# Optimization experiments

Hardware: AMD Instinct MI355X
Metric: run time of the kernel (lower is better)

## Reference

```python
import jax, jax.numpy as jnp
import numpy as np
from jax import lax

N, T, IN = 64, 1024, 64
H = 512
H2 = H // 2   # 256
H4 = H // 4   # 128
H10 = H // 10 # 51


def _lstm(x, Wih, Whh, bih, bhh):
    """PyTorch-style LSTM, batch_first. x: [N,T,in]. Returns hs [N,T,h], h_T, c_T."""
    n, t, _ = x.shape
    h = Whh.shape[1]
    b = bih + bhh

    def step(carry, xt):
        hprev, cprev = carry
        gates = xt @ Wih.T + hprev @ Whh.T + b
        i, f, g, o = jnp.split(gates, 4, axis=-1)
        i = jax.nn.sigmoid(i)
        f = jax.nn.sigmoid(f)
        g = jnp.tanh(g)
        o = jax.nn.sigmoid(o)
        c = f * cprev + i * g
        hnew = o * jnp.tanh(c)
        return (hnew, c), hnew

    h0 = jnp.zeros((n, h), x.dtype)
    c0 = jnp.zeros((n, h), x.dtype)
    (hT, cT), hs = lax.scan(step, (h0, c0), x.transpose(1, 0, 2))
    return hs.transpose(1, 0, 2), hT, cT


def _causal_self_attention(hs):
    """Unscaled dot-product causal attention, equivalent to the python loop."""
    n, t, h = hs.shape
    scores = jnp.einsum('nth,nsh->nts', hs, hs)  # [N,T,T]
    mask = jnp.tril(jnp.ones((t, t), bool))
    scores = jnp.where(mask[None], scores, -jnp.inf)
    attn = jax.nn.softmax(scores, axis=-1)
    return jnp.einsum('nts,nsh->nth', attn, hs)


def setup_inputs() -> dict:
    key = jax.random.key(0)
    ks = jax.random.split(key, 16)
    s = 0.05
    return {
        'x': jax.random.normal(ks[0], (N, T, IN), jnp.float32),
        'W_ih1': jax.random.normal(ks[1], (4 * H, IN), jnp.float32) * s,
        'W_hh1': jax.random.normal(ks[2], (4 * H, H), jnp.float32) * s,
        'b_ih1': jax.random.normal(ks[3], (4 * H,), jnp.float32) * s,
        'b_hh1': jax.random.normal(ks[4], (4 * H,), jnp.float32) * s,
        'W_ih2': jax.random.normal(ks[5], (4 * H2, H), jnp.float32) * s,
        'W_hh2': jax.random.normal(ks[6], (4 * H2, H2), jnp.float32) * s,
        'b_ih2': jax.random.normal(ks[7], (4 * H2,), jnp.float32) * s,
        'b_hh2': jax.random.normal(ks[8], (4 * H2,), jnp.float32) * s,
        'fc1_w': jax.random.normal(ks[9], (H4, 2 * H2), jnp.float32) * s,
        'fc1_b': jax.random.normal(ks[10], (H4,), jnp.float32) * s,
        'fc2_w': jax.random.normal(ks[11], (H10, H4), jnp.float32) * s,
        'fc2_b': jax.random.normal(ks[12], (H10,), jnp.float32) * s,
        'fc3_w': jax.random.normal(ks[13], (1, H10), jnp.float32) * s,
        'fc3_b': jax.random.normal(ks[14], (1,), jnp.float32) * s,
    }


def reference(x, W_ih1, W_hh1, b_ih1, b_hh1, W_ih2, W_hh2, b_ih2, b_hh2,
              fc1_w, fc1_b, fc2_w, fc2_b, fc3_w, fc3_b):
    out, h1, c1 = _lstm(x, W_ih1, W_hh1, b_ih1, b_hh1)     # [N,T,H]
    out, h2, c2 = _lstm(out, W_ih2, W_hh2, b_ih2, b_hh2)   # [N,T,H2]
    contexts = _causal_self_attention(out)                  # [N,T,H2]
    out = jnp.concatenate((contexts, out), axis=2)          # [N,T,2*H2]
    out = jax.nn.relu(out @ fc1_w.T + fc1_b)                # dropout_ratio=0 -> identity
    out = jax.nn.relu(out @ fc2_w.T + fc2_b)
    out = out @ fc3_w.T + fc3_b                              # [N,T,1]
    return out, h1, c1, h2, c2
```

## Files before the change

kernel.cpp:

```cpp
#include <hip/hip_runtime.h>
#include <hip/hip_bf16.h>

#define N_   64
#define T_   1024
#define IN_  64
#define H1_  512
#define H2_  256
#define NG   4
#define NU1  16
#define NU2  8
#define RING 8
#define RING2 4
#define SENT 0xAAAAAAAAu

typedef __bf16 bf16x8 __attribute__((ext_vector_type(8)));
typedef float  f32x4  __attribute__((ext_vector_type(4)));
typedef unsigned int u32x4 __attribute__((ext_vector_type(4)));
typedef unsigned short u16x8 __attribute__((ext_vector_type(8)));
typedef unsigned long long u64;
typedef __hip_bfloat16 bf16_t;

#define OFF_FLG2  8192u
#define OFF_QUE   12288u
#define ZERO_BYTES 16384u
#define OFF_H1R   16384u
#define OFF_H2R   540672u
#define OFF_XB    671744u
#define OFF_W1    9060352u
#define OFF_W2    11419648u
#define OFF_B1    12992512u
#define OFF_B2    13000704u
#define OFF_FC1W  13004800u
#define OFF_FC2W  13135872u
#define OFF_HS2   13152256u
#define OFF_BURN  46706688u

__device__ __forceinline__ bf16x8 ld16(const bf16_t* p) {
  u32x4 u = *reinterpret_cast<const u32x4*>(p);
  return __builtin_bit_cast(bf16x8, u);
}
__device__ __forceinline__ u64 ld64_mall(const void* p) {
  return __hip_atomic_load((const u64*)p, __ATOMIC_RELAXED, __HIP_MEMORY_SCOPE_AGENT);
}
__device__ __forceinline__ void st4_mall(bf16_t* p, unsigned v) {
  __hip_atomic_store((unsigned*)p, v, __ATOMIC_RELAXED, __HIP_MEMORY_SCOPE_AGENT);
}
__device__ __forceinline__ unsigned ldflag(unsigned* p) {
  return __hip_atomic_load(p, __ATOMIC_RELAXED, __HIP_MEMORY_SCOPE_AGENT);
}
__device__ __forceinline__ bool sentok(u64 w) {
  return ((unsigned)w != SENT) && ((unsigned)(w >> 32) != SENT);
}
__device__ __forceinline__ f32x4 mfma_bf16(bf16x8 a, bf16x8 b, f32x4 c) {
  return __builtin_amdgcn_mfma_f32_16x16x32_bf16(a, b, c, 0, 0, 0);
}
__device__ __forceinline__ float sigf(float x) { return 1.f / (1.f + __expf(-x)); }
__device__ __forceinline__ float tanh_fast(float x) {
  float e = __expf(-2.f * fabsf(x));
  float r = (1.f - e) / (1.f + e);
  return x < 0.f ? -r : r;
}
__device__ __forceinline__ unsigned short bf16_bits(float v) {
  __hip_bfloat16 b = __float2bfloat16(v);
  return *reinterpret_cast<unsigned short*>(&b);
}

__global__ void setup_kernel(const float* __restrict__ x,
    const float* __restrict__ Wih1, const float* __restrict__ Whh1,
    const float* __restrict__ bih1, const float* __restrict__ bhh1,
    const float* __restrict__ Wih2, const float* __restrict__ Whh2,
    const float* __restrict__ bih2, const float* __restrict__ bhh2,
    const float* __restrict__ fc1w, const float* __restrict__ fc2w,
    char* __restrict__ ws)
{
  bf16_t* xb = (bf16_t*)(ws + OFF_XB);
  bf16_t* w1 = (bf16_t*)(ws + OFF_W1);
  bf16_t* w2 = (bf16_t*)(ws + OFF_W2);
  float*  b1 = (float*)(ws + OFF_B1);
  float*  b2 = (float*)(ws + OFF_B2);
  bf16_t* f1 = (bf16_t*)(ws + OFF_FC1W);
  bf16_t* f2 = (bf16_t*)(ws + OFF_FC2W);
  const long E0 = 4194304, E1 = E0 + 1179648, E2 = E1 + 786432,
             E3 = E2 + 2048, E4 = E3 + 1024, E5 = E4 + 65536, E6 = E5 + 8192;
  for (long i = blockIdx.x * (long)blockDim.x + threadIdx.x; i < E6;
       i += (long)gridDim.x * blockDim.x) {
    if (i < E0) {
      xb[i] = __float2bfloat16(x[i]);
    } else if (i < E1) {
      long idx = i - E0; long j = idx / 576, k = idx % 576;
      float v = (k < 64) ? Wih1[j * 64 + k] : Whh1[j * 512 + (k - 64)];
      w1[idx] = __float2bfloat16(v);
    } else if (i < E2) {
      long idx = i - E1; long j = idx / 768, k = idx % 768;
      float v = (k < 512) ? Wih2[j * 512 + k] : Whh2[j * 256 + (k - 512)];
      w2[idx] = __float2bfloat16(v);
    } else if (i < E3) {
      long idx = i - E2; b1[idx] = bih1[idx] + bhh1[idx];
    } else if (i < E4) {
      long idx = i - E3; b2[idx] = bih2[idx] + bhh2[idx];
    } else if (i < E5) {
      long idx = i - E4; f1[idx] = __float2bfloat16(fc1w[idx]);
    } else {
      long idx = i - E5; long j = idx / 128, k = idx % 128;
      f2[idx] = __float2bfloat16(j < 51 ? fc2w[j * 128 + k] : 0.f);
    }
  }
}

__global__ __launch_bounds__(256, 1) void fused_kernel(char* __restrict__ ws,
    const float* __restrict__ fc1b, const float* __restrict__ fc2b,
    const float* __restrict__ fc3w, const float* __restrict__ fc3b,
    float* __restrict__ dout)
{
  const bf16_t* xb  = (const bf16_t*)(ws + OFF_XB);
  const bf16_t* W1  = (const bf16_t*)(ws + OFF_W1);
  const bf16_t* W2  = (const bf16_t*)(ws + OFF_W2);
  const float*  b1  = (const float*)(ws + OFF_B1);
  const float*  b2  = (const float*)(ws + OFF_B2);
  bf16_t* h1r = (bf16_t*)(ws + OFF_H1R);
  bf16_t* h2r = (bf16_t*)(ws + OFF_H2R);
  bf16_t* hs2 = (bf16_t*)(ws + OFF_HS2);
  unsigned* flag2 = (unsigned*)(ws + OFF_FLG2);

  __shared__ __align__(16) char smem[55296];

  const int tid  = threadIdx.x;
  const int wave = tid >> 6;
  const int lane = tid & 63;
  const int l15  = lane & 15;
  const int quad = lane >> 4;
  const int bx   = blockIdx.x;
  const f32x4 z = {0.f, 0.f, 0.f, 0.f};

  if (bx < NG * NU1) {
    const int g = bx >> 4, u = bx & 15, u0 = u * 32;
    bf16_t* hstage = (bf16_t*)smem;
    float*  gbuf   = (float*)(smem + 18688);
    bf16x8 wf[18][2];
    #pragma unroll
    for (int i = 0; i < 18; ++i)
      #pragma unroll
      for (int nt = 0; nt < 2; ++nt)
        wf[i][nt] = ld16(W1 + (size_t)(wave * H1_ + u0 + nt * 16 + l15) * 576 + i * 32 + quad * 8);

    const int sr = tid >> 4;
    const int myp = tid & 15;
    const int row = tid >> 4, ui = (tid & 15) * 2;
    const int nrow = g * 16 + row;
    unsigned* bp = flag2 + (g * NU2 + (tid & 7)) * 32;
    float bi[2], bff[2], bg[2], bo[2], creg[2];
    #pragma unroll
    for (int j = 0; j < 2; ++j) {
      int ug = u0 + ui + j;
      bi[j]  = b1[ug];         bff[j] = b1[H1_ + ug];
      bg[j]  = b1[2*H1_ + ug]; bo[j]  = b1[3*H1_ + ug];
      creg[j] = 0.f;
    }
    #pragma unroll
    for (int s = 0; s < RING; ++s)
      st4_mall(h1r + ((size_t)(g * RING + s) * 16 + row) * 512 + u0 + ui, SENT);

    #pragma unroll 1
    for (int t = 0; t < T_; ++t) {
      {
        u64 xv = *(const u64*)(xb + ((size_t)(g*16 + sr) * T_ + t) * IN_ + myp * 4);
        *(u64*)(hstage + sr * 584 + myp * 4) = xv;
      }
      if (t >= 7)
        while ((int)ldflag(bp) < t - 6) __builtin_amdgcn_s_sleep(1);
      if (t == 0) {
        #pragma unroll
        for (int k = 0; k < 8; ++k)
          *(u64*)(hstage + sr * 584 + 64 + myp * 32 + k * 4) = 0ull;
      } else {
        const u64* src = (const u64*)(h1r + ((size_t)(g * RING + ((t-1) & 7)) * 16 + sr) * 512 + myp * 32);
        u64 w[8];
        for (;;) {
          #pragma unroll
          for (int k = 0; k < 8; ++k) w[k] = ld64_mall(src + k);
          bool ok = true;
          #pragma unroll
          for (int k = 0; k < 8; ++k) ok &= sentok(w[k]);
          if (ok) break;
        }
        #pragma unroll
        for (int k = 0; k < 8; ++k)
          *(u64*)(hstage + sr * 584 + 64 + myp * 32 + k * 4) = w[k];
      }
      __syncthreads();
      st4_mall(h1r + ((size_t)(g * RING + ((t+1) & 7)) * 16 + row) * 512 + u0 + ui, SENT);
      f32x4 acc[2] = {z, z}, acd[2] = {z, z};
      #pragma unroll
      for (int ki = 0; ki < 9; ++ki) {
        bf16x8 aw = ld16(hstage + l15 * 584 + ki * 32 + quad * 8);
        acc[0] = mfma_bf16(aw, wf[ki][0], acc[0]);
        acc[1] = mfma_bf16(aw, wf[ki][1], acc[1]);
      }
      #pragma unroll
      for (int ki = 9; ki < 18; ++ki) {
        bf16x8 aw = ld16(hstage + l15 * 584 + ki * 32 + quad * 8);
        acd[0] = mfma_bf16(aw, wf[ki][0], acd[0]);
        acd[1] = mfma_bf16(aw, wf[ki][1], acd[1]);
      }
      acc[0] += acd[0]; acc[1] += acd[1];
      #pragma unroll
      for (int nt = 0; nt < 2; ++nt)
        #pragma unroll
        for (int r = 0; r < 4; ++r)
          gbuf[(wave * 16 + quad * 4 + r) * 33 + nt * 16 + l15] = acc[nt][r];
      __syncthreads();
      {
        unsigned pack = 0;
        float hv[2];
        #pragma unroll
        for (int j = 0; j < 2; ++j) {
          int col = ui + j;
          float iv = sigf(gbuf[(0*16 + row) * 33 + col] + bi[j]);
          float fv = sigf(gbuf[(1*16 + row) * 33 + col] + bff[j]);
          float gv = tanh_fast(gbuf[(2*16 + row) * 33 + col] + bg[j]);
          float ov = sigf(gbuf[(3*16 + row) * 33 + col] + bo[j]);
          float c = fv * creg[j] + iv * gv;
          creg[j] = c;
          float h = ov * tanh_fast(c);
          hv[j] = h;
          pack |= (unsigned)bf16_bits(h) << (16 * j);
        }
        st4_mall(h1r + ((size_t)(g * RING + (t & 7)) * 16 + row) * 512 + u0 + ui, pack);
        if (t == T_ - 1) {
          #pragma unroll
          for (int j = 0; j < 2; ++j) {
            dout[65536 + nrow * H1_ + u0 + ui + j] = hv[j];
            dout[98304 + nrow * H1_ + u0 + ui + j] = creg[j];
          }
        }
      }
    }
  } else if (bx < NG * NU1 + NG * NU2) {
    const int b2x = bx - NG * NU1;
    const int g = b2x >> 3, u = b2x & 7, u0 = u * 32;
    bf16_t* hstage = (bf16_t*)smem;
    float*  gbuf   = (float*)(smem + 25088);
    bf16x8 wf[24][2];
    #pragma unroll
    for (int i = 0; i < 24; ++i)
      #pragma unroll
      for (int nt = 0; nt < 2; ++nt)
        wf[i][nt] = ld16(W2 + (size_t)(wave * H2_ + u0 + nt * 16 + l15) * 768 + i * 32 + quad * 8);

    const int sr = tid >> 4;
    const int q  = tid & 15;
    const int row = tid >> 4, ui = (tid & 15) * 2;
    const int nrow = g * 16 + row;
    unsigned* myflag = flag2 + (g * NU2 + u) * 32;
    float bi[2], bff[2], bg[2], bo[2], creg[2];
    #pragma unroll
    for (int j = 0; j < 2; ++j) {
      int ug = u0 + ui + j;
      bi[j]  = b2[ug];         bff[j] = b2[H2_ + ug];
      bg[j]  = b2[2*H2_ + ug]; bo[j]  = b2[3*H2_ + ug];
      creg[j] = 0.f;
    }
    #pragma unroll
    for (int s = 0; s < RING2; ++s)
      st4_mall(h2r + ((size_t)(g * RING2 + s) * 16 + row) * 256 + u0 + ui, SENT);

    u64 pf[8];
    #pragma unroll 1
    for (int t = 0; t < T_; ++t) {
      {
        const u64* s1 = (const u64*)(h1r + ((size_t)(g * RING + (t & 7)) * 16 + sr) * 512 + q * 32);
        bool good = (t > 0);
        if (good) {
          #pragma unroll
          for (int k = 0; k < 8; ++k) good &= sentok(pf[k]);
        }
        if (!good) {
          for (;;) {
            #pragma unroll
            for (int k = 0; k < 8; ++k) pf[k] = ld64_mall(s1 + k);
            bool ok = true;
            #pragma unroll
            for (int k = 0; k < 8; ++k) ok &= sentok(pf[k]);
            if (ok) break;
          }
        }
        #pragma unroll
        for (int k = 0; k < 8; ++k)
          *(u64*)(hstage + sr * 784 + q * 32 + k * 4) = pf[k];
      }
      if (t == 0) {
        #pragma unroll
        for (int k = 0; k < 4; ++k)
          *(u64*)(hstage + sr * 784 + 512 + q * 16 + k * 4) = 0ull;
      } else {
        const u64* s2 = (const u64*)(h2r + ((size_t)(g * RING2 + ((t-1) & 3)) * 16 + sr) * 256 + q * 16);
        u64 w[4];
        for (;;) {
          #pragma unroll
          for (int k = 0; k < 4; ++k) w[k] = ld64_mall(s2 + k);
          bool ok = true;
          #pragma unroll
          for (int k = 0; k < 4; ++k) ok &= sentok(w[k]);
          if (ok) break;
        }
        #pragma unroll
        for (int k = 0; k < 4; ++k)
          *(u64*)(hstage + sr * 784 + 512 + q * 16 + k * 4) = w[k];
      }
      __syncthreads();
      if (tid == 0 && t > 0)
        __hip_atomic_store(myflag, (unsigned)t, __ATOMIC_RELAXED, __HIP_MEMORY_SCOPE_AGENT);
      st4_mall(h2r + ((size_t)(g * RING2 + ((t+1) & 3)) * 16 + row) * 256 + u0 + ui, SENT);
      f32x4 acc[2] = {z, z}, acd[2] = {z, z};
      #pragma unroll
      for (int ki = 0; ki < 12; ++ki) {
        bf16x8 aw = ld16(hstage + l15 * 784 + ki * 32 + quad * 8);
        acc[0] = mfma_bf16(aw, wf[ki][0], acc[0]);
        acc[1] = mfma_bf16(aw, wf[ki][1], acc[1]);
      }
      #pragma unroll
      for (int ki = 12; ki < 24; ++ki) {
        bf16x8 aw = ld16(hstage + l15 * 784 + ki * 32 + quad * 8);
        acd[0] = mfma_bf16(aw, wf[ki][0], acd[0]);
        acd[1] = mfma_bf16(aw, wf[ki][1], acd[1]);
      }
      acc[0] += acd[0]; acc[1] += acd[1];
      #pragma unroll
      for (int nt = 0; nt < 2; ++nt)
        #pragma unroll
        for (int r = 0; r < 4; ++r)
          gbuf[(wave * 16 + quad * 4 + r) * 33 + nt * 16 + l15] = acc[nt][r];
      __syncthreads();
      {
        unsigned pack = 0;
        float hv[2];
        #pragma unroll
        for (int j = 0; j < 2; ++j) {
          int col = ui + j;
          float iv = sigf(gbuf[(0*16 + row) * 33 + col] + bi[j]);
          float fv = sigf(gbuf[(1*16 + row) * 33 + col] + bff[j]);
          float gv = tanh_fast(gbuf[(2*16 + row) * 33 + col] + bg[j]);
          float ov = sigf(gbuf[(3*16 + row) * 33 + col] + bo[j]);
          float c = fv * creg[j] + iv * gv;
          creg[j] = c;
          float h = ov * tanh_fast(c);
          hv[j] = h;
          pack |= (unsigned)bf16_bits(h) << (16 * j);
        }
        st4_mall(h2r + ((size_t)(g * RING2 + (t & 3)) * 16 + row) * 256 + u0 + ui, pack);
        st4_mall(hs2 + ((size_t)nrow * T_ + t) * H2_ + u0 + ui, pack);
        if (t == T_ - 1) {
          #pragma unroll
          for (int j = 0; j < 2; ++j) {
            dout[131072 + nrow * H2_ + u0 + ui + j] = hv[j];
            dout[147456 + nrow * H2_ + u0 + ui + j] = creg[j];
          }
        }
      }
      if (t + 1 < T_) {
        const u64* nx = (const u64*)(h1r + ((size_t)(g * RING + ((t+1) & 7)) * 16 + sr) * 512 + q * 32);
        #pragma unroll
        for (int k = 0; k < 8; ++k) pf[k] = ld64_mall(nx + k);
      }
    }
    __syncthreads();
    if (tid == 0)
      __hip_atomic_store(myflag, (unsigned)T_, __ATOMIC_RELAXED, __HIP_MEMORY_SCOPE_AGENT);
  }

  __syncthreads();
  {
    const bf16_t* f1w = (const bf16_t*)(ws + OFF_FC1W);
    const bf16_t* f2w = (const bf16_t*)(ws + OFF_FC2W);
    unsigned* queue = (unsigned*)(ws + OFF_QUE);
    unsigned short* vtile = (unsigned short*)smem;
    bf16_t* plds   = (bf16_t*)(smem + 36864);
    bf16_t* ctxlds = (bf16_t*)smem;
    bf16_t* act1   = (bf16_t*)(smem + 36864);
    float*  act2   = (float*)smem;
    volatile int* itemslot = (volatile int*)(smem + 55040);
    float burn = 1.0f;

    for (;;) {
      if (tid == 0) *itemslot = (int)atomicAdd(queue, 1u);
      __syncthreads();
      const int item = *itemslot;
      __syncthreads();
      if (item >= 1024) break;
      const int qt = item >> 6, n = item & 63, q0 = qt * 64, gg = n >> 4;

      {
        const int need = q0 + 64;
        if (tid < 64) {
          unsigned* p = (lane < NU2) ? flag2 + (gg * NU2 + lane) * 32 : nullptr;
          bool ok = (p == nullptr) || ((int)ldflag(p) >= need);
          while (!__all(ok)) {
            #pragma unroll
            for (int k = 0; k < 32; ++k) burn = fmaf(burn, 1.0000001f, 1e-7f);
            ok = (p == nullptr) || ((int)ldflag(p) >= need);
          }
        }
        __syncthreads();
      }

      bf16x8 aq[8];
      #pragma unroll
      for (int ks = 0; ks < 8; ++ks)
        aq[ks] = ld16(hs2 + ((size_t)n * T_ + q0 + wave * 16 + l15) * H2_ + ks * 32 + quad * 8);
      f32x4 o[16];
      #pragma unroll
      for (int ct = 0; ct < 16; ++ct) o[ct] = z;
      float m_run[4], l_run[4];
      #pragma unroll
      for (int r = 0; r < 4; ++r) { m_run[r] = -1e30f; l_run[r] = 0.f; }
      bf16_t* pw = plds + wave * 1152;

      #pragma unroll 1
      for (int st = 0; st <= qt; ++st) {
        const int s0 = st * 64;
        __syncthreads();
        #pragma unroll
        for (int it = 0; it < 8; ++it) {
          int s  = (tid >> 3) + (it & 1) * 32;
          int c0 = (tid & 7) * 8 + (it >> 1) * 64;
          u16x8 v = *reinterpret_cast<const u16x8*>(
              (const unsigned short*)hs2 + ((size_t)n * T_ + s0 + s) * H2_ + c0);
          #pragma unroll
          for (int j = 0; j < 8; ++j) {
            int ch = c0 + j;
            int sw = (s & 7) | ((((s >> 3) ^ (ch >> 3)) & 7) << 3);
            vtile[ch * 72 + sw] = v[j];
          }
        }
        __syncthreads();
        f32x4 sc[4] = {z, z, z, z};
        #pragma unroll
        for (int ks = 0; ks < 8; ++ks) {
          #pragma unroll
          for (int nt = 0; nt < 4; ++nt) {
            bf16x8 bk = ld16(hs2 + ((size_t)n * T_ + s0 + nt * 16 + l15) * H2_ + ks * 32 + quad * 8);
            sc[nt] = mfma_bf16(aq[ks], bk, sc[nt]);
          }
        }
        if (st == qt) {
          int qg = q0 + wave * 16 + quad * 4;
          #pragma unroll
          for (int nt = 0; nt < 4; ++nt) {
            int sg = s0 + nt * 16 + l15;
            #pragma unroll
            for (int r = 0; r < 4; ++r)
              if (sg > qg + r) sc[nt][r] = -1e30f;
          }
        }
        float alpha[4];
        #pragma unroll
        for (int r = 0; r < 4; ++r) {
          float tm = fmaxf(fmaxf(sc[0][r], sc[1][r]), fmaxf(sc[2][r], sc[3][r]));
          tm = fmaxf(tm, __shfl_xor(tm, 1, 16));
          tm = fmaxf(tm, __shfl_xor(tm, 2, 16));
          tm = fmaxf(tm, __shfl_xor(tm, 4, 16));
          tm = fmaxf(tm, __shfl_xor(tm, 8, 16));
          float mnew = fmaxf(m_run[r], tm);
          alpha[r] = __expf(m_run[r] - mnew);
          m_run[r] = mnew;
          float ts = 0.f;
          #pragma unroll
          for (int nt = 0; nt < 4; ++nt) {
            float p = __expf(sc[nt][r] - mnew);
            sc[nt][r] = p;
            ts += p;
          }
          ts += __shfl_xor(ts, 1, 16);
          ts += __shfl_xor(ts, 2, 16);
          ts += __shfl_xor(ts, 4, 16);
          ts += __shfl_xor(ts, 8, 16);
          l_run[r] = l_run[r] * alpha[r] + ts;
        }
        #pragma unroll
        for (int ct = 0; ct < 16; ++ct)
          #pragma unroll
          for (int r = 0; r < 4; ++r)
            o[ct][r] *= alpha[r];
        #pragma unroll
        for (int nt = 0; nt < 4; ++nt)
          #pragma unroll
          for (int r = 0; r < 4; ++r)
            pw[(quad * 4 + r) * 72 + nt * 16 + l15] = __float2bfloat16(sc[nt][r]);
        #pragma unroll
        for (int ks2 = 0; ks2 < 2; ++ks2) {
          bf16x8 ap = ld16(pw + l15 * 72 + ks2 * 32 + quad * 8);
          #pragma unroll
          for (int ct = 0; ct < 16; ++ct) {
            int ch = ct * 16 + l15;
            int blk = ((ks2 * 4 + quad) ^ (ch >> 3)) & 7;
            bf16x8 bv = ld16((bf16_t*)vtile + ch * 72 + blk * 8);
            o[ct] = mfma_bf16(ap, bv, o[ct]);
          }
        }
      }
      __syncthreads();
      float inv[4];
      #pragma unroll
      for (int r = 0; r < 4; ++r) inv[r] = 1.f / l_run[r];
      #pragma unroll
      for (int ct = 0; ct < 16; ++ct)
        #pragma unroll
        for (int r = 0; r < 4; ++r)
          ctxlds[(wave * 16 + quad * 4 + r) * 264 + ct * 16 + l15] =
              __float2bfloat16(o[ct][r] * inv[r]);
      __syncthreads();

      f32x4 a1[4][2];
      #pragma unroll
      for (int mt = 0; mt < 4; ++mt) { a1[mt][0] = z; a1[mt][1] = z; }
      #pragma unroll
      for (int ks = 0; ks < 16; ++ks) {
        bf16x8 af[4];
        if (ks < 8) {
          #pragma unroll
          for (int mt = 0; mt < 4; ++mt)
            af[mt] = ld16(ctxlds + (mt * 16 + l15) * 264 + ks * 32 + quad * 8);
        } else {
          #pragma unroll
          for (int mt = 0; mt < 4; ++mt)
            af[mt] = ld16(hs2 + ((size_t)n * T_ + q0 + mt * 16 + l15) * H2_ + (ks - 8) * 32 + quad * 8);
        }
        #pragma unroll
        for (int nt = 0; nt < 2; ++nt) {
          bf16x8 bw = ld16(f1w + (size_t)(wave * 32 + nt * 16 + l15) * 512 + ks * 32 + quad * 8);
          #pragma unroll
          for (int mt = 0; mt < 4; ++mt)
            a1[mt][nt] = mfma_bf16(af[mt], bw, a1[mt][nt]);
        }
      }
      #pragma unroll
      for (int mt = 0; mt < 4; ++mt)
        #pragma unroll
        for (int nt = 0; nt < 2; ++nt)
          #pragma unroll
          for (int r = 0; r < 4; ++r) {
            int ch = wave * 32 + nt * 16 + l15;
            float v = a1[mt][nt][r] + fc1b[ch];
            act1[(mt * 16 + quad * 4 + r) * 136 + ch] = __float2bfloat16(fmaxf(v, 0.f));
          }
      __syncthreads();

      f32x4 a2[4] = {z, z, z, z};
      #pragma unroll
      for (int ks = 0; ks < 4; ++ks) {
        bf16x8 bw = ld16(f2w + (wave * 16 + l15) * 128 + ks * 32 + quad * 8);
        #pragma unroll
        for (int mt = 0; mt < 4; ++mt) {
          bf16x8 af = ld16(act1 + (mt * 16 + l15) * 136 + ks * 32 + quad * 8);
          a2[mt] = mfma_bf16(af, bw, a2[mt]);
        }
      }
      __syncthreads();
      #pragma unroll
      for (int mt = 0; mt < 4; ++mt)
        #pragma unroll
        for (int r = 0; r < 4; ++r) {
          int ch = wave * 16 + l15;
          int rw = mt * 16 + quad * 4 + r;
          float v = a2[mt][r] + (ch < 51 ? fc2b[ch] : 0.f);
          act2[rw * 68 + ch] = fmaxf(v, 0.f);
        }
      __syncthreads();
      if (tid < 64) {
        float s = fc3b[0];
        for (int c = 0; c < 51; ++c) s += act2[tid * 68 + c] * fc3w[c];
        dout[(size_t)n * T_ + q0 + tid] = s;
      }
      __syncthreads();
    }
    if (burn == 0.1234567f)
      ((float*)(ws + OFF_BURN))[tid] = burn;
  }
}

extern "C" void kernel_launch(void* const* d_in, const int* in_sizes, int n_in,
                              void* d_out, int out_size, void* d_ws, size_t ws_size,
                              hipStream_t stream) {
  (void)in_sizes; (void)n_in; (void)out_size; (void)ws_size;
  const float* x    = (const float*)d_in[0];
  const float* Wih1 = (const float*)d_in[1];
  const float* Whh1 = (const float*)d_in[2];
  const float* bih1 = (const float*)d_in[3];
  const float* bhh1 = (const float*)d_in[4];
  const float* Wih2 = (const float*)d_in[5];
  const float* Whh2 = (const float*)d_in[6];
  const float* bih2 = (const float*)d_in[7];
  const float* bhh2 = (const float*)d_in[8];
  const float* fc1w = (const float*)d_in[9];
  const float* fc1b = (const float*)d_in[10];
  const float* fc2w = (const float*)d_in[11];
  const float* fc2b = (const float*)d_in[12];
  const float* fc3w = (const float*)d_in[13];
  const float* fc3b = (const float*)d_in[14];
  char* ws  = (char*)d_ws;
  float* out = (float*)d_out;

  hipMemsetAsync(ws, 0, ZERO_BYTES, stream);
  setup_kernel<<<2048, 256, 0, stream>>>(x, Wih1, Whh1, bih1, bhh1,
                                         Wih2, Whh2, bih2, bhh2, fc1w, fc2w, ws);
  fused_kernel<<<256, 256, 0, stream>>>(ws, fc1b, fc2b, fc3w, fc3b, out);
}
```

Measured before the change: 3.108 ms.

## Fuse LSTM layer 2 into layer-1 blocks with one-step skewed pipeline

Removes the separate layer-2 block group. Each of the 64 layer-1 blocks now also computes 16 layer-2 hidden units, one timestep behind layer 1, reusing the h1 already staged in LDS as layer-2 input. This drops the cross-block handoff of h1 to layer-2 blocks and the backpressure flag wait in layer 1, and frees CUs for the attention stage. In exchange each block runs more MFMAs per step, holds more weight registers, and the layer-2 h2 exchange now spans 16 blocks per group. The burn loop in the attention wait is also lengthened.

```diff
diff --git a/kernel.cpp b/kernel.cpp
--- a/kernel.cpp
+++ b/kernel.cpp
@@ -7,8 +7,7 @@
 #define H1_  512
 #define H2_  256
 #define NG   4
-#define NU1  16
-#define NU2  8
+#define NLB  16
 #define RING 8
 #define RING2 4
 #define SENT 0xAAAAAAAAu
@@ -20,7 +19,7 @@
 typedef unsigned long long u64;
 typedef __hip_bfloat16 bf16_t;
 
-#define OFF_FLG2  8192u
+#define OFF_FLGP  0u
 #define OFF_QUE   12288u
 #define ZERO_BYTES 16384u
 #define OFF_H1R   16384u
@@ -120,7 +119,7 @@
   bf16_t* h1r = (bf16_t*)(ws + OFF_H1R);
   bf16_t* h2r = (bf16_t*)(ws + OFF_H2R);
   bf16_t* hs2 = (bf16_t*)(ws + OFF_HS2);
-  unsigned* flag2 = (unsigned*)(ws + OFF_FLG2);
+  unsigned* flagP = (unsigned*)(ws + OFF_FLGP);
 
   __shared__ __align__(16) char smem[55296];
 
@@ -132,95 +131,165 @@
   const int bx   = blockIdx.x;
   const f32x4 z = {0.f, 0.f, 0.f, 0.f};
 
-  if (bx < NG * NU1) {
-    const int g = bx >> 4, u = bx & 15, u0 = u * 32;
-    bf16_t* hstage = (bf16_t*)smem;
-    float*  gbuf   = (float*)(smem + 18688);
-    bf16x8 wf[18][2];
+  if (bx < NG * NLB) {
+    const int g = bx >> 4, u = bx & 15, u0 = u * 32, u02 = u * 16;
+    bf16_t* hstage  = (bf16_t*)smem;
+    bf16_t* h2stage = (bf16_t*)(smem + 18688);
+    float*  gbuf1   = (float*)(smem + 27136);
+    float*  gbuf2   = (float*)(smem + 35584);
+
+    bf16x8 wf1[18][2];
     #pragma unroll
     for (int i = 0; i < 18; ++i)
       #pragma unroll
       for (int nt = 0; nt < 2; ++nt)
-        wf[i][nt] = ld16(W1 + (size_t)(wave * H1_ + u0 + nt * 16 + l15) * 576 + i * 32 + quad * 8);
+        wf1[i][nt] = ld16(W1 + (size_t)(wave * H1_ + u0 + nt * 16 + l15) * 576 + i * 32 + quad * 8);
+    bf16x8 wf2[24];
+    #pragma unroll
+    for (int i = 0; i < 24; ++i)
+      wf2[i] = ld16(W2 + (size_t)(wave * H2_ + u02 + l15) * 768 + i * 32 + quad * 8);
 
     const int sr = tid >> 4;
     const int myp = tid & 15;
-    const int row = tid >> 4, ui = (tid & 15) * 2;
+    const int row = sr, ui = myp * 2;
+    const int unit2 = myp;
     const int nrow = g * 16 + row;
-    unsigned* bp = flag2 + (g * NU2 + (tid & 7)) * 32;
-    float bi[2], bff[2], bg[2], bo[2], creg[2];
+    unsigned* myflag = flagP + (g * NLB + u) * 32;
+
+    float b1i[2], b1f[2], b1g[2], b1o[2], creg1[2];
     #pragma unroll
     for (int j = 0; j < 2; ++j) {
       int ug = u0 + ui + j;
-      bi[j]  = b1[ug];         bff[j] = b1[H1_ + ug];
-      bg[j]  = b1[2*H1_ + ug]; bo[j]  = b1[3*H1_ + ug];
-      creg[j] = 0.f;
+      b1i[j] = b1[ug];          b1f[j] = b1[H1_ + ug];
+      b1g[j] = b1[2*H1_ + ug];  b1o[j] = b1[3*H1_ + ug];
+      creg1[j] = 0.f;
     }
+    float b2i, b2f, b2g, b2o, creg2 = 0.f;
+    { int ug2 = u02 + unit2;
+      b2i = b2[ug2]; b2f = b2[H2_ + ug2]; b2g = b2[2*H2_ + ug2]; b2o = b2[3*H2_ + ug2]; }
+
     #pragma unroll
     for (int s = 0; s < RING; ++s)
       st4_mall(h1r + ((size_t)(g * RING + s) * 16 + row) * 512 + u0 + ui, SENT);
-
+    if (!(tid & 1))
+      #pragma unroll
+      for (int s = 0; s < RING2; ++s)
+        st4_mall(h2r + ((size_t)(g * RING2 + s) * 16 + row) * 256 + u02 + unit2, SENT);
+
+    u64 pf1[8], pf2[4];
     #pragma unroll 1
-    for (int t = 0; t < T_; ++t) {
-      {
+    for (int t = 0; t <= T_; ++t) {
+      if (t < T_) {
         u64 xv = *(const u64*)(xb + ((size_t)(g*16 + sr) * T_ + t) * IN_ + myp * 4);
         *(u64*)(hstage + sr * 584 + myp * 4) = xv;
       }
-      if (t >= 7)
-        while ((int)ldflag(bp) < t - 6) __builtin_amdgcn_s_sleep(1);
       if (t == 0) {
         #pragma unroll
         for (int k = 0; k < 8; ++k)
           *(u64*)(hstage + sr * 584 + 64 + myp * 32 + k * 4) = 0ull;
       } else {
-        const u64* src = (const u64*)(h1r + ((size_t)(g * RING + ((t-1) & 7)) * 16 + sr) * 512 + myp * 32);
-        u64 w[8];
-        for (;;) {
-          #pragma unroll
-          for (int k = 0; k < 8; ++k) w[k] = ld64_mall(src + k);
-          bool ok = true;
-          #pragma unroll
-          for (int k = 0; k < 8; ++k) ok &= sentok(w[k]);
-          if (ok) break;
+        const u64* s1 = (const u64*)(h1r + ((size_t)(g * RING + ((t-1) & 7)) * 16 + sr) * 512 + myp * 32);
+        bool good = true;
+        #pragma unroll
+        for (int k = 0; k < 8; ++k) good &= sentok(pf1[k]);
+        if (!good) {
+          for (;;) {
+            #pragma unroll
+            for (int k = 0; k < 8; ++k) pf1[k] = ld64_mall(s1 + k);
+            bool ok = true;
+            #pragma unroll
+            for (int k = 0; k < 8; ++k) ok &= sentok(pf1[k]);
+            if (ok) break;
+          }
         }
         #pragma unroll
         for (int k = 0; k < 8; ++k)
-          *(u64*)(hstage + sr * 584 + 64 + myp * 32 + k * 4) = w[k];
-      }
-      __syncthreads();
-      st4_mall(h1r + ((size_t)(g * RING + ((t+1) & 7)) * 16 + row) * 512 + u0 + ui, SENT);
-      f32x4 acc[2] = {z, z}, acd[2] = {z, z};
-      #pragma unroll
-      for (int ki = 0; ki < 9; ++ki) {
-        bf16x8 aw = ld16(hstage + l15 * 584 + ki * 32 + quad * 8);
-        acc[0] = mfma_bf16(aw, wf[ki][0], acc[0]);
-        acc[1] = mfma_bf16(aw, wf[ki][1], acc[1]);
-      }
-      #pragma unroll
-      for (int ki = 9; ki < 18; ++ki) {
-        bf16x8 aw = ld16(hstage + l15 * 584 + ki * 32 + quad * 8);
-        acd[0] = mfma_bf16(aw, wf[ki][0], acd[0]);
-        acd[1] = mfma_bf16(aw, wf[ki][1], acd[1]);
-      }
-      acc[0] += acd[0]; acc[1] += acd[1];
-      #pragma unroll
-      for (int nt = 0; nt < 2; ++nt)
+          *(u64*)(hstage + sr * 584 + 64 + myp * 32 + k * 4) = pf1[k];
+      }
+      if (t >= 2) {
+        const u64* s2 = (const u64*)(h2r + ((size_t)(g * RING2 + ((t-2) & 3)) * 16 + sr) * 256 + myp * 16);
+        bool good = true;
+        #pragma unroll
+        for (int k = 0; k < 4; ++k) good &= sentok(pf2[k]);
+        if (!good) {
+          for (;;) {
+            #pragma unroll
+            for (int k = 0; k < 4; ++k) pf2[k] = ld64_mall(s2 + k);
+            bool ok = true;
+            #pragma unroll
+            for (int k = 0; k < 4; ++k) ok &= sentok(pf2[k]);
+            if (ok) break;
+          }
+        }
+        #pragma unroll
+        for (int k = 0; k < 4; ++k)
+          *(u64*)(h2stage + sr * 264 + myp * 16 + k * 4) = pf2[k];
+      } else if (t == 1) {
+        #pragma unroll
+        for (int k = 0; k < 4; ++k)
+          *(u64*)(h2stage + sr * 264 + myp * 16 + k * 4) = 0ull;
+      }
+      __syncthreads();
+      if (tid == 0 && t >= 2)
+        __hip_atomic_store(myflag, (unsigned)(t - 1), __ATOMIC_RELAXED, __HIP_MEMORY_SCOPE_AGENT);
+      if (t < T_) {
+        st4_mall(h1r + ((size_t)(g * RING + ((t+1) & 7)) * 16 + row) * 512 + u0 + ui, SENT);
+        if (!(tid & 1))
+          st4_mall(h2r + ((size_t)(g * RING2 + ((t+1) & 3)) * 16 + row) * 256 + u02 + unit2, SENT);
+      }
+      if (t < T_) {
+        f32x4 acc[2] = {z, z}, acd[2] = {z, z};
+        #pragma unroll
+        for (int ki = 0; ki < 9; ++ki) {
+          bf16x8 aw = ld16(hstage + l15 * 584 + ki * 32 + quad * 8);
+          acc[0] = mfma_bf16(aw, wf1[ki][0], acc[0]);
+          acc[1] = mfma_bf16(aw, wf1[ki][1], acc[1]);
+        }
+        #pragma unroll
+        for (int ki = 9; ki < 18; ++ki) {
+          bf16x8 aw = ld16(hstage + l15 * 584 + ki * 32 + quad * 8);
+          acd[0] = mfma_bf16(aw, wf1[ki][0], acd[0]);
+          acd[1] = mfma_bf16(aw, wf1[ki][1], acd[1]);
+        }
+        acc[0] += acd[0]; acc[1] += acd[1];
+        #pragma unroll
+        for (int nt = 0; nt < 2; ++nt)
+          #pragma unroll
+          for (int r = 0; r < 4; ++r)
+            gbuf1[(wave * 16 + quad * 4 + r) * 33 + nt * 16 + l15] = acc[nt][r];
+      }
+      if (t >= 1) {
+        f32x4 a2a = z, a2b = z;
+        #pragma unroll
+        for (int ki = 0; ki < 12; ++ki) {
+          bf16x8 aw = ld16(hstage + l15 * 584 + 64 + ki * 32 + quad * 8);
+          a2a = mfma_bf16(aw, wf2[ki], a2a);
+        }
+        #pragma unroll
+        for (int ki = 12; ki < 24; ++ki) {
+          bf16x8 aw = (ki < 16)
+              ? ld16(hstage + l15 * 584 + 64 + ki * 32 + quad * 8)
+              : ld16(h2stage + l15 * 264 + (ki - 16) * 32 + quad * 8);
+          a2b = mfma_bf16(aw, wf2[ki], a2b);
+        }
+        a2a += a2b;
         #pragma unroll
         for (int r = 0; r < 4; ++r)
-          gbuf[(wave * 16 + quad * 4 + r) * 33 + nt * 16 + l15] = acc[nt][r];
-      __syncthreads();
-      {
+          gbuf2[(wave * 16 + quad * 4 + r) * 17 + l15] = a2a[r];
+      }
+      __syncthreads();
+      if (t < T_) {
         unsigned pack = 0;
         float hv[2];
         #pragma unroll
         for (int j = 0; j < 2; ++j) {
           int col = ui + j;
-          float iv = sigf(gbuf[(0*16 + row) * 33 + col] + bi[j]);
-          float fv = sigf(gbuf[(1*16 + row) * 33 + col] + bff[j]);
-          float gv = tanh_fast(gbuf[(2*16 + row) * 33 + col] + bg[j]);
-          float ov = sigf(gbuf[(3*16 + row) * 33 + col] + bo[j]);
-          float c = fv * creg[j] + iv * gv;
-          creg[j] = c;
+          float iv = sigf(gbuf1[(0*16 + row) * 33 + col] + b1i[j]);
+          float fv = sigf(gbuf1[(1*16 + row) * 33 + col] + b1f[j]);
+          float gv = tanh_fast(gbuf1[(2*16 + row) * 33 + col] + b1g[j]);
+          float ov = sigf(gbuf1[(3*16 + row) * 33 + col] + b1o[j]);
+          float c = fv * creg1[j] + iv * gv;
+          creg1[j] = c;
           float h = ov * tanh_fast(c);
           hv[j] = h;
           pack |= (unsigned)bf16_bits(h) << (16 * j);
@@ -230,137 +299,40 @@
           #pragma unroll
           for (int j = 0; j < 2; ++j) {
             dout[65536 + nrow * H1_ + u0 + ui + j] = hv[j];
-            dout[98304 + nrow * H1_ + u0 + ui + j] = creg[j];
-          }
-        }
-      }
-    }
-  } else if (bx < NG * NU1 + NG * NU2) {
-    const int b2x = bx - NG * NU1;
-    const int g = b2x >> 3, u = b2x & 7, u0 = u * 32;
-    bf16_t* hstage = (bf16_t*)smem;
-    float*  gbuf   = (float*)(smem + 25088);
-    bf16x8 wf[24][2];
-    #pragma unroll
-    for (int i = 0; i < 24; ++i)
-      #pragma unroll
-      for (int nt = 0; nt < 2; ++nt)
-        wf[i][nt] = ld16(W2 + (size_t)(wave * H2_ + u0 + nt * 16 + l15) * 768 + i * 32 + quad * 8);
-
-    const int sr = tid >> 4;
-    const int q  = tid & 15;
-    const int row = tid >> 4, ui = (tid & 15) * 2;
-    const int nrow = g * 16 + row;
-    unsigned* myflag = flag2 + (g * NU2 + u) * 32;
-    float bi[2], bff[2], bg[2], bo[2], creg[2];
-    #pragma unroll
-    for (int j = 0; j < 2; ++j) {
-      int ug = u0 + ui + j;
-      bi[j]  = b2[ug];         bff[j] = b2[H2_ + ug];
-      bg[j]  = b2[2*H2_ + ug]; bo[j]  = b2[3*H2_ + ug];
-      creg[j] = 0.f;
-    }
-    #pragma unroll
-    for (int s = 0; s < RING2; ++s)
-      st4_mall(h2r + ((size_t)(g * RING2 + s) * 16 + row) * 256 + u0 + ui, SENT);
-
-    u64 pf[8];
-    #pragma unroll 1
-    for (int t = 0; t < T_; ++t) {
-      {
-        const u64* s1 = (const u64*)(h1r + ((size_t)(g * RING + (t & 7)) * 16 + sr) * 512 + q * 32);
-        bool good = (t > 0);
-        if (good) {
-          #pragma unroll
-          for (int k = 0; k < 8; ++k) good &= sentok(pf[k]);
-        }
-        if (!good) {
-          for (;;) {
-            #pragma unroll
-            for (int k = 0; k < 8; ++k) pf[k] = ld64_mall(s1 + k);
-            bool ok = true;
-            #pragma unroll
-            for (int k = 0; k < 8; ++k) ok &= sentok(pf[k]);
-            if (ok) break;
-          }
-        }
-        #pragma unroll
-        for (int k = 0; k < 8; ++k)
-          *(u64*)(hstage + sr * 784 + q * 32 + k * 4) = pf[k];
-      }
-      if (t == 0) {
-        #pragma unroll
-        for (int k = 0; k < 4; ++k)
-          *(u64*)(hstage + sr * 784 + 512 + q * 16 + k * 4) = 0ull;
-      } else {
-        const u64* s2 = (const u64*)(h2r + ((size_t)(g * RING2 + ((t-1) & 3)) * 16 + sr) * 256 + q * 16);
-        u64 w[4];
-        for (;;) {
-          #pragma unroll
-          for (int k = 0; k < 4; ++k) w[k] = ld64_mall(s2 + k);
-          bool ok = true;
-          #pragma unroll
-          for (int k = 0; k < 4; ++k) ok &= sentok(w[k]);
-          if (ok) break;
-        }
-        #pragma unroll
-        for (int k = 0; k < 4; ++k)
-          *(u64*)(hstage + sr * 784 + 512 + q * 16 + k * 4) = w[k];
-      }
-      __syncthreads();
-      if (tid == 0 && t > 0)
-        __hip_atomic_store(myflag, (unsigned)t, __ATOMIC_RELAXED, __HIP_MEMORY_SCOPE_AGENT);
-      st4_mall(h2r + ((size_t)(g * RING2 + ((t+1) & 3)) * 16 + row) * 256 + u0 + ui, SENT);
-      f32x4 acc[2] = {z, z}, acd[2] = {z, z};
-      #pragma unroll
-      for (int ki = 0; ki < 12; ++ki) {
-        bf16x8 aw = ld16(hstage + l15 * 784 + ki * 32 + quad * 8);
-        acc[0] = mfma_bf16(aw, wf[ki][0], acc[0]);
-        acc[1] = mfma_bf16(aw, wf[ki][1], acc[1]);
-      }
-      #pragma unroll
-      for (int ki = 12; ki < 24; ++ki) {
-        bf16x8 aw = ld16(hstage + l15 * 784 + ki * 32 + quad * 8);
-        acd[0] = mfma_bf16(aw, wf[ki][0], acd[0]);
-        acd[1] = mfma_bf16(aw, wf[ki][1], acd[1]);
-      }
-      acc[0] += acd[0]; acc[1] += acd[1];
-      #pragma unroll
-      for (int nt = 0; nt < 2; ++nt)
-        #pragma unroll
-        for (int r = 0; r < 4; ++r)
-          gbuf[(wave * 16 + quad * 4 + r) * 33 + nt * 16 + l15] = acc[nt][r];
-      __syncthreads();
-      {
-        unsigned pack = 0;
-        float hv[2];
-        #pragma unroll
-        for (int j = 0; j < 2; ++j) {
-          int col = ui + j;
-          float iv = sigf(gbuf[(0*16 + row) * 33 + col] + bi[j]);
-          float fv = sigf(gbuf[(1*16 + row) * 33 + col] + bff[j]);
-          float gv = tanh_fast(gbuf[(2*16 + row) * 33 + col] + bg[j]);
-          float ov = sigf(gbuf[(3*16 + row) * 33 + col] + bo[j]);
-          float c = fv * creg[j] + iv * gv;
-          creg[j] = c;
-          float h = ov * tanh_fast(c);
-          hv[j] = h;
-          pack |= (unsigned)bf16_bits(h) << (16 * j);
-        }
-        st4_mall(h2r + ((size_t)(g * RING2 + (t & 3)) * 16 + row) * 256 + u0 + ui, pack);
-        st4_mall(hs2 + ((size_t)nrow * T_ + t) * H2_ + u0 + ui, pack);
-        if (t == T_ - 1) {
-          #pragma unroll
-          for (int j = 0; j < 2; ++j) {
-            dout[131072 + nrow * H2_ + u0 + ui + j] = hv[j];
-            dout[147456 + nrow * H2_ + u0 + ui + j] = creg[j];
-          }
-        }
-      }
-      if (t + 1 < T_) {
-        const u64* nx = (const u64*)(h1r + ((size_t)(g * RING + ((t+1) & 7)) * 16 + sr) * 512 + q * 32);
-        #pragma unroll
-        for (int k = 0; k < 8; ++k) pf[k] = ld64_mall(nx + k);
+            dout[98304 + nrow * H1_ + u0 + ui + j] = creg1[j];
+          }
+        }
+      }
+      if (t >= 1) {
+        const int tm1 = t - 1;
+        float iv = sigf(gbuf2[(0*16 + row) * 17 + unit2] + b2i);
+        float fv = sigf(gbuf2[(1*16 + row) * 17 + unit2] + b2f);
+        float gv = tanh_fast(gbuf2[(2*16 + row) * 17 + unit2] + b2g);
+        float ov = sigf(gbuf2[(3*16 + row) * 17 + unit2] + b2o);
+        float c2 = fv * creg2 + iv * gv;
+        creg2 = c2;
+        float h2v = ov * tanh_fast(c2);
+        unsigned mb = bf16_bits(h2v);
+        unsigned ob = __shfl_xor(mb, 1);
+        if (!(tid & 1)) {
+          unsigned pk = mb | (ob << 16);
+          st4_mall(h2r + ((size_t)(g * RING2 + (tm1 & 3)) * 16 + row) * 256 + u02 + unit2, pk);
+          st4_mall(hs2 + ((size_t)nrow * T_ + tm1) * H2_ + u02 + unit2, pk);
+        }
+        if (tm1 == T_ - 1) {
+          dout[131072 + nrow * H2_ + u02 + unit2] = h2v;
+          dout[147456 + nrow * H2_ + u02 + unit2] = creg2;
+        }
+      }
+      if (t < T_) {
+        const u64* nx1 = (const u64*)(h1r + ((size_t)(g * RING + (t & 7)) * 16 + sr) * 512 + myp * 32);
+        #pragma unroll
+        for (int k = 0; k < 8; ++k) pf1[k] = ld64_mall(nx1 + k);
+        if (t >= 1) {
+          const u64* nx2 = (const u64*)(h2r + ((size_t)(g * RING2 + ((t-1) & 3)) * 16 + sr) * 256 + myp * 16);
+          #pragma unroll
+          for (int k = 0; k < 4; ++k) pf2[k] = ld64_mall(nx2 + k);
+        }
       }
     }
     __syncthreads();
@@ -392,11 +364,11 @@
       {
         const int need = q0 + 64;
         if (tid < 64) {
-          unsigned* p = (lane < NU2) ? flag2 + (gg * NU2 + lane) * 32 : nullptr;
+          unsigned* p = (lane < NLB) ? flagP + (gg * NLB + lane) * 32 : nullptr;
           bool ok = (p == nullptr) || ((int)ldflag(p) >= need);
           while (!__all(ok)) {
             #pragma unroll
-            for (int k = 0; k < 32; ++k) burn = fmaf(burn, 1.0000001f, 1e-7f);
+            for (int k = 0; k < 128; ++k) burn = fmaf(burn, 1.0000001f, 1e-7f);
             ok = (p == nullptr) || ((int)ldflag(p) >= need);
           }
         }
```

Result: slower. 4.532 ms (+45.8%).
